# Optimization experiments

Measured on AMD Instinct MI355X. Metric: run time of the kernel, lower is better.

The kernel has to match this reference:

```python
import jax, jax.numpy as jnp
import numpy as np

LATTICE_SIZE = 3
LATTICE_RANK = 4
NUM_LATTICES = 1024
NUM_FEATURES = 128
BATCH = 2048
NUM_VERTICES = LATTICE_SIZE ** LATTICE_RANK  # 81


def _rtl_indices(seed=42):
    # Randomized feature->lattice arrangement: each lattice gets LATTICE_RANK
    # distinct features (every input column is its own group, so the
    # group-avoidance constraint reduces to 'distinct features per lattice').
    rng = np.random.default_rng(seed)
    idx = np.argsort(rng.random((NUM_LATTICES, NUM_FEATURES)), axis=1)[:, :LATTICE_RANK]
    return jnp.asarray(idx, dtype=jnp.int32)


def setup_inputs() -> dict:
    key = jax.random.key(0)
    k1, k2 = jax.random.split(key)
    # Calibrated inputs live in the lattice input range [0, lattice_size - 1].
    x = jax.random.uniform(k1, (BATCH, NUM_FEATURES), dtype=jnp.float32) * (LATTICE_SIZE - 1)
    # random_monotonic_initializer: uniform in [output_min, output_max] = [0, 1].
    kernel = jax.random.uniform(k2, (NUM_VERTICES, NUM_LATTICES), dtype=jnp.float32)
    indices = _rtl_indices()
    return {"x": x, "kernel": kernel, "indices": indices}


def reference(x, kernel, indices):
    s = LATTICE_SIZE
    # Group-aware gather: assemble per-lattice inputs. (B, L, R)
    xg = jnp.clip(x[:, indices], 0.0, s - 1.0)  # clip_inputs=True
    verts = jnp.arange(s, dtype=x.dtype)  # (s,)
    # Per-dimension hypercube (multilinear) interpolation weights: (B, L, R, s)
    w = jnp.maximum(jnp.float32(0.0), 1.0 - jnp.abs(xg[..., None] - verts))
    B, L = xg.shape[0], xg.shape[1]
    # Outer product over rank dims -> full vertex weights (B, L, s**R)
    W = w[:, :, 0, :]
    for r in range(1, LATTICE_RANK):
        W = (W[..., :, None] * w[:, :, r][:, :, None, :]).reshape(B, L, -1)
    # Per-lattice matvec against lattice vertex parameters.
    out = jnp.einsum('blv,vl->bl', W, kernel)  # (B, num_lattices)
    return out
```

## Files before the change

### kernel.cpp

```cpp
#include <hip/hip_runtime.h>


#define BATCH   2048
#define NFEAT   128
#define NLAT    1024
#define NVERT   81
#define LT      128
#define BT      32
#define THREADS 256

__global__ __launch_bounds__(THREADS, 2)
void rtl_kernel(const float* __restrict__ x,
                const float* __restrict__ kern,
                const int*   __restrict__ indices,
                float*       __restrict__ out) {
    __shared__ float Klds[NVERT * LT];
    __shared__ float Xlds[BT * NFEAT];

    const int tid   = threadIdx.x;
    const int ltile = blockIdx.x & (NLAT / LT - 1);
    const int btile = blockIdx.x >> 3;
    const int l0    = ltile * LT;
    const int b0    = btile * BT;

    {
        float4* dst4 = (float4*)Klds;
        for (int i = tid; i < NVERT * (LT / 4); i += THREADS) {
            const int v = i >> 5;
            const int c = i & 31;
            dst4[i] = *(const float4*)(kern + v * NLAT + l0 + c * 4);
        }
    }
    {
        float4* dst4 = (float4*)Xlds;
        const float4* src4 = (const float4*)(x + b0 * NFEAT);
        for (int i = tid; i < (BT * NFEAT) / 4; i += THREADS) {
            dst4[i] = src4[i];
        }
    }

    const int ll   = tid & (LT - 1);
    const int bsub = tid >> 7;
    const int4 idx = *(const int4*)(indices + (l0 + ll) * 4);

    __syncthreads();

    const float* kbase = Klds + ll;

    for (int bi = bsub; bi < BT; bi += THREADS / LT) {
        const float* xr = Xlds + bi * NFEAT;
        float x0 = xr[idx.x];
        float x1 = xr[idx.y];
        float x2 = xr[idx.z];
        float x3 = xr[idx.w];
        x0 = fminf(fmaxf(x0, 0.0f), 2.0f);
        x1 = fminf(fmaxf(x1, 0.0f), 2.0f);
        x2 = fminf(fmaxf(x2, 0.0f), 2.0f);
        x3 = fminf(fmaxf(x3, 0.0f), 2.0f);
        const int i0 = min((int)x0, 1); const float t0 = x0 - (float)i0;
        const int i1 = min((int)x1, 1); const float t1 = x1 - (float)i1;
        const int i2 = min((int)x2, 1); const float t2 = x2 - (float)i2;
        const int i3 = min((int)x3, 1); const float t3 = x3 - (float)i3;

        const int vb = ((i0 * 3 + i1) * 3 + i2) * 3 + i3;
        const float* kp = kbase + vb * LT;

        float a3[8];
#pragma unroll
        for (int c = 0; c < 8; ++c) {
            const int d = ((c >> 2) & 1) * 27 + ((c >> 1) & 1) * 9 + (c & 1) * 3;
            const float lo = kp[d * LT];
            const float hi = kp[(d + 1) * LT];
            a3[c] = fmaf(t3, hi - lo, lo);
        }
        float a2[4];
#pragma unroll
        for (int j = 0; j < 4; ++j) {
            a2[j] = fmaf(t2, a3[2 * j + 1] - a3[2 * j], a3[2 * j]);
        }
        const float n0 = fmaf(t1, a2[1] - a2[0], a2[0]);
        const float n1 = fmaf(t1, a2[3] - a2[2], a2[2]);
        const float res = fmaf(t0, n1 - n0, n0);

        out[(b0 + bi) * NLAT + l0 + ll] = res;
    }
}

extern "C" void kernel_launch(void* const* d_in, const int* in_sizes, int n_in,
                              void* d_out, int out_size, void* d_ws, size_t ws_size,
                              hipStream_t stream) {
    const float* x       = (const float*)d_in[0];
    const float* kern    = (const float*)d_in[1];
    const int*   indices = (const int*)d_in[2];
    float*       out     = (float*)d_out;

    const int grid = (NLAT / LT) * (BATCH / BT);
    rtl_kernel<<<grid, THREADS, 0, stream>>>(x, kern, indices, out);
}
```

Before: 13.42 us.

## Pack lattice vertex quads into float4 LDS and read x directly from global

Restructures the kernel parameter staging so each LDS float4 holds the 2x2 (i2,i3) vertex quad, replacing 16 scalar LDS reads per output with 4 float4 reads. The lattice tile shrinks to 64 with one wavefront per lattice lane set, and the x tile is no longer staged in LDS but gathered straight from global/cache. Launch bounds go to 4 blocks per CU. The quad layout duplicates vertices (36 quads x 4 = 144 floats vs 81), adding redundant global loads during staging, and uncoalesced global gathers of x may cost latency.

```diff
diff --git a/kernel.cpp b/kernel.cpp
--- a/kernel.cpp
+++ b/kernel.cpp
@@ -1,88 +1,86 @@
 #include <hip/hip_runtime.h>
 
 
-#define BATCH   2048
 #define NFEAT   128
 #define NLAT    1024
-#define NVERT   81
-#define LT      128
+#define BATCH   2048
+#define LT      64
 #define BT      32
 #define THREADS 256
+#define NQUAD   36
 
-__global__ __launch_bounds__(THREADS, 2)
+__global__ __launch_bounds__(THREADS, 4)
 void rtl_kernel(const float* __restrict__ x,
                 const float* __restrict__ kern,
                 const int*   __restrict__ indices,
                 float*       __restrict__ out) {
-    __shared__ float Klds[NVERT * LT];
-    __shared__ float Xlds[BT * NFEAT];
+    __shared__ float4 Kq[NQUAD * LT];
 
     const int tid   = threadIdx.x;
-    const int ltile = blockIdx.x & (NLAT / LT - 1);
-    const int btile = blockIdx.x >> 3;
+    const int ltile = blockIdx.x & 15;
+    const int btile = blockIdx.x >> 4;
     const int l0    = ltile * LT;
     const int b0    = btile * BT;
 
-    {
-        float4* dst4 = (float4*)Klds;
-        for (int i = tid; i < NVERT * (LT / 4); i += THREADS) {
-            const int v = i >> 5;
-            const int c = i & 31;
-            dst4[i] = *(const float4*)(kern + v * NLAT + l0 + c * 4);
-        }
-    }
-    {
-        float4* dst4 = (float4*)Xlds;
-        const float4* src4 = (const float4*)(x + b0 * NFEAT);
-        for (int i = tid; i < (BT * NFEAT) / 4; i += THREADS) {
-            dst4[i] = src4[i];
-        }
+    for (int i = tid; i < NQUAD * LT; i += THREADS) {
+        const int q  = i >> 6;
+        const int l  = i & (LT - 1);
+        const int m  = q >> 2;
+        const int jj = q & 3;
+        const int u  = 9 * m + 3 * (jj >> 1) + (jj & 1);
+        const float* kp = kern + u * NLAT + l0 + l;
+        Kq[i] = make_float4(kp[0], kp[NLAT], kp[3 * NLAT], kp[4 * NLAT]);
     }
 
-    const int ll   = tid & (LT - 1);
-    const int bsub = tid >> 7;
-    const int4 idx = *(const int4*)(indices + (l0 + ll) * 4);
+    const int lane = tid & 63;
+    const int wid  = __builtin_amdgcn_readfirstlane(tid >> 6);
+    const int4 idx = *(const int4*)(indices + (l0 + lane) * 4);
 
     __syncthreads();
 
-    const float* kbase = Klds + ll;
+    const float4* col = Kq + lane;
 
-    for (int bi = bsub; bi < BT; bi += THREADS / LT) {
-        const float* xr = Xlds + bi * NFEAT;
-        float x0 = xr[idx.x];
-        float x1 = xr[idx.y];
-        float x2 = xr[idx.z];
-        float x3 = xr[idx.w];
-        x0 = fminf(fmaxf(x0, 0.0f), 2.0f);
-        x1 = fminf(fmaxf(x1, 0.0f), 2.0f);
-        x2 = fminf(fmaxf(x2, 0.0f), 2.0f);
-        x3 = fminf(fmaxf(x3, 0.0f), 2.0f);
-        const int i0 = min((int)x0, 1); const float t0 = x0 - (float)i0;
-        const int i1 = min((int)x1, 1); const float t1 = x1 - (float)i1;
-        const int i2 = min((int)x2, 1); const float t2 = x2 - (float)i2;
-        const int i3 = min((int)x3, 1); const float t3 = x3 - (float)i3;
+#pragma unroll 2
+    for (int k = 0; k < 8; ++k) {
+        const int bi = wid * 8 + k;
+        const float* xr = x + (b0 + bi) * NFEAT;
 
-        const int vb = ((i0 * 3 + i1) * 3 + i2) * 3 + i3;
-        const float* kp = kbase + vb * LT;
+        float x0 = fminf(fmaxf(xr[idx.x], 0.0f), 2.0f);
+        float x1 = fminf(fmaxf(xr[idx.y], 0.0f), 2.0f);
+        float x2 = fminf(fmaxf(xr[idx.z], 0.0f), 2.0f);
+        float x3 = fminf(fmaxf(xr[idx.w], 0.0f), 2.0f);
 
-        float a3[8];
-#pragma unroll
-        for (int c = 0; c < 8; ++c) {
-            const int d = ((c >> 2) & 1) * 27 + ((c >> 1) & 1) * 9 + (c & 1) * 3;
-            const float lo = kp[d * LT];
-            const float hi = kp[(d + 1) * LT];
-            a3[c] = fmaf(t3, hi - lo, lo);
-        }
-        float a2[4];
-#pragma unroll
-        for (int j = 0; j < 4; ++j) {
-            a2[j] = fmaf(t2, a3[2 * j + 1] - a3[2 * j], a3[2 * j]);
-        }
-        const float n0 = fmaf(t1, a2[1] - a2[0], a2[0]);
-        const float n1 = fmaf(t1, a2[3] - a2[2], a2[2]);
+        const int  i0 = (x0 >= 1.0f);  const float t0 = x0 - (float)i0;
+        const int  i1 = (x1 >= 1.0f);  const float t1 = x1 - (float)i1;
+        const int  i2 = (x2 >= 1.0f);  const float t2 = x2 - (float)i2;
+        const int  i3 = (x3 >= 1.0f);  const float t3 = x3 - (float)i3;
+
+        const int q00 = 12 * i0 + 4 * i1 + 2 * i2 + i3;
+        const float4* cq = col + q00 * LT;
+
+        const float4 fA = cq[0];
+        const float4 fB = cq[4 * LT];
+        const float4 fC = cq[12 * LT];
+        const float4 fD = cq[16 * LT];
+
+        const float eA0 = fmaf(t3, fA.y - fA.x, fA.x);
+        const float eA1 = fmaf(t3, fA.w - fA.z, fA.z);
+        const float cA  = fmaf(t2, eA1 - eA0, eA0);
+        const float eB0 = fmaf(t3, fB.y - fB.x, fB.x);
+        const float eB1 = fmaf(t3, fB.w - fB.z, fB.z);
+        const float cB  = fmaf(t2, eB1 - eB0, eB0);
+        const float eC0 = fmaf(t3, fC.y - fC.x, fC.x);
+        const float eC1 = fmaf(t3, fC.w - fC.z, fC.z);
+        const float cC  = fmaf(t2, eC1 - eC0, eC0);
+        const float eD0 = fmaf(t3, fD.y - fD.x, fD.x);
+        const float eD1 = fmaf(t3, fD.w - fD.z, fD.z);
+        const float cD  = fmaf(t2, eD1 - eD0, eD0);
+
+        const float n0  = fmaf(t1, cB - cA, cA);
+        const float n1  = fmaf(t1, cD - cC, cC);
         const float res = fmaf(t0, n1 - n0, n0);
 
-        out[(b0 + bi) * NLAT + l0 + ll] = res;
+        out[(b0 + bi) * NLAT + l0 + lane] = res;
     }
 }
 
```

Result: slower. 14.06 us (+4.8%).
